# Performance work log

Measured on AMD Instinct MI355X. Metric: run time of the kernel, lower is better.

Reference implementation:

```python
import jax, jax.numpy as jnp
import numpy as np

N = 50000        # nodes
E = 800000       # edges (avg degree 16)
H = 128          # hidden_channels
R = 6            # num_radial
SH = 3           # spin_hidden_channels


def _linear_params(key, out_dim, in_dim):
    # torch Linear default init: U(-1/sqrt(in), 1/sqrt(in)) for weight and bias
    kw, kb = jax.random.split(key)
    bound = 1.0 / np.sqrt(in_dim)
    W = jax.random.uniform(kw, (out_dim, in_dim), minval=-bound, maxval=bound, dtype=jnp.float32)
    b = jax.random.uniform(kb, (out_dim,), minval=-bound, maxval=bound, dtype=jnp.float32)
    return W, b


def setup_inputs() -> dict:
    key = jax.random.key(0)
    ks = jax.random.split(key, 9)
    x = jax.random.randint(ks[0], (N,), 0, 95)                       # atom types
    s = jax.random.randint(ks[1], (N,), 0, 3)                        # spin class in {0,1,2} == (spin + 1)
    rbf = jax.random.normal(ks[2], (E, R), dtype=jnp.float32)
    i = jax.random.randint(ks[3], (E,), 0, N)
    j = jax.random.randint(ks[4], (E,), 0, N)
    emb_w = jax.random.uniform(ks[5], (95, H), minval=-np.sqrt(3), maxval=np.sqrt(3), dtype=jnp.float32)
    spin_w, spin_b = _linear_params(ks[6], SH, 3)
    rbf_w, rbf_b = _linear_params(ks[7], H, R)
    lin_w, lin_b = _linear_params(ks[8], H, 3 * H + 2 * SH)
    return {"x": x, "s": s, "rbf": rbf, "i": i, "j": j,
            "emb_w": emb_w, "spin_w": spin_w, "spin_b": spin_b,
            "rbf_w": rbf_w, "rbf_b": rbf_b, "lin_w": lin_w, "lin_b": lin_b}


def reference(x, s, rbf, i, j, emb_w, spin_w, spin_b, rbf_w, rbf_b, lin_w, lin_b):
    act = jax.nn.silu
    h = emb_w[x]                                              # [N, H] embedding lookup
    spin_oh = jax.nn.one_hot(s, 3, dtype=spin_w.dtype)        # [N, 3]
    spin_feat = spin_oh @ spin_w.T + spin_b                   # [N, SH]
    r = act(rbf @ rbf_w.T + rbf_b)                            # [E, H]
    # concat order matches torch: [x_i, spin_i, x_j, spin_j, rbf]
    feat = jnp.concatenate([h[i], spin_feat[i], h[j], spin_feat[j], r], axis=-1)  # [E, 3H+2SH]
    return act(feat @ lin_w.T + lin_b)                        # [E, H]
```

## Files before the change

### kernel.cpp

```cpp
#include <hip/hip_runtime.h>
#include <hip/hip_bf16.h>

#define NH   128
#define NR   6
#define NCOL 390
#define TILE_E 64
#define LDK  136

typedef __attribute__((ext_vector_type(8))) short bf16x8;
typedef __attribute__((ext_vector_type(4))) float f32x4;

__global__ void prep_tables(const float* __restrict__ emb_w,
                            const float* __restrict__ spin_w,
                            const float* __restrict__ spin_b,
                            const float* __restrict__ lin_w,
                            const float* __restrict__ lin_b,
                            float* __restrict__ Ci, float* __restrict__ Cj) {
    int row = blockIdx.x;
    int n   = threadIdx.x;
    bool isJ = row >= 285;
    int rr = isJ ? row - 285 : row;
    int a  = rr / 3;
    int sc = rr % 3;
    const int col0 = isJ ? 131 : 0;
    const int cols = isJ ? 259 : 128;
    const float* wrow = lin_w + (size_t)n * NCOL;
    float acc = isJ ? 0.0f : lin_b[n];
    #pragma unroll 8
    for (int k = 0; k < NH; ++k)
        acc += emb_w[a * NH + k] * wrow[col0 + k];
    #pragma unroll
    for (int c = 0; c < 3; ++c)
        acc += (spin_w[c * 3 + sc] + spin_b[c]) * wrow[cols + c];
    (isJ ? Cj : Ci)[rr * NH + n] = acc;
}

__global__ void prep_w(const float* __restrict__ lin_w, __hip_bfloat16* __restrict__ Wb) {
    int idx = blockIdx.x * 256 + threadIdx.x;
    int n = idx >> 7, k = idx & 127;
    Wb[idx] = __float2bfloat16(lin_w[(size_t)n * NCOL + 262 + k]);
}

__global__ __launch_bounds__(256, 2) void fused_main(
        const int*   __restrict__ x,   const int* __restrict__ s,
        const float* __restrict__ rbf,
        const int*   __restrict__ gi,  const int* __restrict__ gj,
        const float* __restrict__ rbf_w, const float* __restrict__ rbf_b,
        const float* __restrict__ Ci,  const float* __restrict__ Cj,
        const __hip_bfloat16* __restrict__ Wb,
        float* __restrict__ out, int E) {
    __shared__ __align__(16) __hip_bfloat16 r_lds[TILE_E * LDK];
    __shared__ __align__(16) __hip_bfloat16 w_lds[NH * LDK];
    __shared__ float rbf_lds[TILE_E * NR];
    __shared__ int ci_lds[TILE_E], cj_lds[TILE_E];

    const int tid = threadIdx.x;
    const int e0  = blockIdx.x * TILE_E;

    {
        const uint4* src = (const uint4*)Wb;
        #pragma unroll
        for (int it = 0; it < 8; ++it) {
            int l = it * 256 + tid;
            int row = l >> 4, c = l & 15;
            uint4 v = src[l];
            *(uint4*)&w_lds[row * LDK + c * 8] = v;
        }
    }

    if (tid < 192) {
        int nvalid = (E - e0 >= TILE_E ? TILE_E : (E - e0)) * NR;
        float2 v = make_float2(0.f, 0.f);
        if (tid * 2 < nvalid)
            v = ((const float2*)(rbf + (size_t)e0 * NR))[tid];
        ((float2*)rbf_lds)[tid] = v;
    }

    if (tid < TILE_E) {
        int e = e0 + tid; if (e >= E) e = E - 1;
        int ii = gi[e];
        ci_lds[tid] = x[ii] * 3 + s[ii];
    } else if (tid < 2 * TILE_E) {
        int t = tid - TILE_E;
        int e = e0 + t; if (e >= E) e = E - 1;
        int jj = gj[e];
        cj_lds[t] = x[jj] * 3 + s[jj];
    }
    __syncthreads();

    {
        int k  = tid & 127;
        int hi = tid >> 7;
        float w0 = rbf_w[k * NR + 0], w1 = rbf_w[k * NR + 1], w2 = rbf_w[k * NR + 2];
        float w3 = rbf_w[k * NR + 3], w4 = rbf_w[k * NR + 4], w5 = rbf_w[k * NR + 5];
        float bb = rbf_b[k];
        #pragma unroll 4
        for (int t = 0; t < 32; ++t) {
            int e = t * 2 + hi;
            const float* re = &rbf_lds[e * NR];
            float acc = bb + re[0] * w0 + re[1] * w1 + re[2] * w2
                           + re[3] * w3 + re[4] * w4 + re[5] * w5;
            float sv = acc / (1.0f + __expf(-acc));
            r_lds[e * LDK + k] = __float2bfloat16(sv);
        }
    }
    __syncthreads();

    const int wave   = tid >> 6;
    const int lane   = tid & 63;
    const int lane15 = lane & 15;
    const int quad   = lane >> 4;
    const int e_sub  = wave * 16;

    bf16x8 afrag[4];
    #pragma unroll
    for (int kt = 0; kt < 4; ++kt)
        afrag[kt] = *(const bf16x8*)&r_lds[(e_sub + lane15) * LDK + kt * 32 + quad * 8];

    const int e_row = e_sub + quad * 4;
    int cio[4], cjo[4];
    #pragma unroll
    for (int reg = 0; reg < 4; ++reg) {
        cio[reg] = ci_lds[e_row + reg] * NH;
        cjo[reg] = cj_lds[e_row + reg] * NH;
    }

    #pragma unroll
    for (int nt = 0; nt < 8; ++nt) {
        f32x4 acc = {0.f, 0.f, 0.f, 0.f};
        #pragma unroll
        for (int kt = 0; kt < 4; ++kt) {
            bf16x8 bfrag = *(const bf16x8*)&w_lds[(nt * 16 + lane15) * LDK + kt * 32 + quad * 8];
            acc = __builtin_amdgcn_mfma_f32_16x16x32_bf16(afrag[kt], bfrag, acc, 0, 0, 0);
        }
        int n = nt * 16 + lane15;
        #pragma unroll
        for (int reg = 0; reg < 4; ++reg) {
            int eg = e0 + e_row + reg;
            if (eg < E) {
                float base = Ci[cio[reg] + n] + Cj[cjo[reg] + n];
                float v = acc[reg] + base;
                out[(size_t)eg * NH + n] = v / (1.0f + __expf(-v));
            }
        }
    }
}

extern "C" void kernel_launch(void* const* d_in, const int* in_sizes, int n_in,
                              void* d_out, int out_size, void* d_ws, size_t ws_size,
                              hipStream_t stream) {
    const int*   x      = (const int*)  d_in[0];
    const int*   s      = (const int*)  d_in[1];
    const float* rbf    = (const float*)d_in[2];
    const int*   gi     = (const int*)  d_in[3];
    const int*   gj     = (const int*)  d_in[4];
    const float* emb_w  = (const float*)d_in[5];
    const float* spin_w = (const float*)d_in[6];
    const float* spin_b = (const float*)d_in[7];
    const float* rbf_w  = (const float*)d_in[8];
    const float* rbf_b  = (const float*)d_in[9];
    const float* lin_w  = (const float*)d_in[10];
    const float* lin_b  = (const float*)d_in[11];
    const int E = in_sizes[3];

    float* Ci = (float*)d_ws;
    float* Cj = Ci + 285 * NH;
    __hip_bfloat16* Wb = (__hip_bfloat16*)(Cj + 285 * NH);

    prep_tables<<<570, 128, 0, stream>>>(emb_w, spin_w, spin_b, lin_w, lin_b, Ci, Cj);
    prep_w<<<64, 256, 0, stream>>>(lin_w, Wb);

    int nblk = (E + TILE_E - 1) / TILE_E;
    fused_main<<<nblk, 256, 0, stream>>>(x, s, rbf, gi, gj, rbf_w, rbf_b,
                                         Ci, Cj, Wb, (float*)d_out, E);
}
```

Baseline: 690.4 us.

## Make fused edge kernel persistent with prefetch of next tile's inputs

Converts the main kernel into a persistent grid-stride loop over 128-edge tiles with 512-thread blocks. The bf16 weight tile and rbf weights now load once per block rather than once per tile, and the next tile's rbf values and gathered node indices are prefetched into registers while MFMA and epilogue run. It also uses a reciprocal-based SiLU and nontemporal output stores. Risks are the extra syncs per tile and lower parallelism from a fixed 512-block grid, plus register pressure at 512 threads.

```diff
diff --git a/kernel.cpp b/kernel.cpp
--- a/kernel.cpp
+++ b/kernel.cpp
@@ -4,11 +4,16 @@
 #define NH   128
 #define NR   6
 #define NCOL 390
-#define TILE_E 64
+#define TILE_E 128
 #define LDK  136
+#define NBLK 512
 
 typedef __attribute__((ext_vector_type(8))) short bf16x8;
 typedef __attribute__((ext_vector_type(4))) float f32x4;
+
+__device__ __forceinline__ float fast_silu(float v) {
+    return v * __builtin_amdgcn_rcpf(1.0f + __expf(-v));
+}
 
 __global__ void prep_tables(const float* __restrict__ emb_w,
                             const float* __restrict__ spin_w,
@@ -41,106 +46,122 @@
     Wb[idx] = __float2bfloat16(lin_w[(size_t)n * NCOL + 262 + k]);
 }
 
-__global__ __launch_bounds__(256, 2) void fused_main(
+__global__ __launch_bounds__(512, 4) void fused_main(
         const int*   __restrict__ x,   const int* __restrict__ s,
         const float* __restrict__ rbf,
         const int*   __restrict__ gi,  const int* __restrict__ gj,
         const float* __restrict__ rbf_w, const float* __restrict__ rbf_b,
         const float* __restrict__ Ci,  const float* __restrict__ Cj,
         const __hip_bfloat16* __restrict__ Wb,
-        float* __restrict__ out, int E) {
+        float* __restrict__ out, int E, int ntiles) {
+    __shared__ __align__(16) __hip_bfloat16 w_lds[NH * LDK];
     __shared__ __align__(16) __hip_bfloat16 r_lds[TILE_E * LDK];
-    __shared__ __align__(16) __hip_bfloat16 w_lds[NH * LDK];
     __shared__ float rbf_lds[TILE_E * NR];
     __shared__ int ci_lds[TILE_E], cj_lds[TILE_E];
 
     const int tid = threadIdx.x;
-    const int e0  = blockIdx.x * TILE_E;
+
+    float2 srbf = make_float2(0.f, 0.f);
+    int sci = 0, scj = 0;
+
+    auto load_tile = [&](int tt) {
+        const int en0 = tt * TILE_E;
+        if (tid < 384) {
+            int nval = (E - en0 >= TILE_E ? TILE_E : E - en0) * NR;
+            float2 v = make_float2(0.f, 0.f);
+            if (tid * 2 < nval)
+                v = ((const float2*)(rbf + (size_t)en0 * NR))[tid];
+            srbf = v;
+        }
+        if (tid >= 384) {
+            int e = en0 + (tid - 384); if (e >= E) e = E - 1;
+            int ii = gi[e];
+            sci = x[ii] * 3 + s[ii];
+        }
+        if (tid < 128) {
+            int e = en0 + tid; if (e >= E) e = E - 1;
+            int jj = gj[e];
+            scj = x[jj] * 3 + s[jj];
+        }
+    };
+
+    const int t0 = blockIdx.x;
+    const int gstride = gridDim.x;
+    load_tile(t0);
 
     {
         const uint4* src = (const uint4*)Wb;
         #pragma unroll
-        for (int it = 0; it < 8; ++it) {
-            int l = it * 256 + tid;
-            int row = l >> 4, c = l & 15;
+        for (int it = 0; it < 4; ++it) {
+            int l = it * 512 + tid;
             uint4 v = src[l];
-            *(uint4*)&w_lds[row * LDK + c * 8] = v;
+            *(uint4*)&w_lds[(l >> 4) * LDK + (l & 15) * 8] = v;
         }
     }
 
-    if (tid < 192) {
-        int nvalid = (E - e0 >= TILE_E ? TILE_E : (E - e0)) * NR;
-        float2 v = make_float2(0.f, 0.f);
-        if (tid * 2 < nvalid)
-            v = ((const float2*)(rbf + (size_t)e0 * NR))[tid];
-        ((float2*)rbf_lds)[tid] = v;
-    }
-
-    if (tid < TILE_E) {
-        int e = e0 + tid; if (e >= E) e = E - 1;
-        int ii = gi[e];
-        ci_lds[tid] = x[ii] * 3 + s[ii];
-    } else if (tid < 2 * TILE_E) {
-        int t = tid - TILE_E;
-        int e = e0 + t; if (e >= E) e = E - 1;
-        int jj = gj[e];
-        cj_lds[t] = x[jj] * 3 + s[jj];
-    }
-    __syncthreads();
-
-    {
-        int k  = tid & 127;
-        int hi = tid >> 7;
-        float w0 = rbf_w[k * NR + 0], w1 = rbf_w[k * NR + 1], w2 = rbf_w[k * NR + 2];
-        float w3 = rbf_w[k * NR + 3], w4 = rbf_w[k * NR + 4], w5 = rbf_w[k * NR + 5];
-        float bb = rbf_b[k];
-        #pragma unroll 4
-        for (int t = 0; t < 32; ++t) {
-            int e = t * 2 + hi;
-            const float* re = &rbf_lds[e * NR];
-            float acc = bb + re[0] * w0 + re[1] * w1 + re[2] * w2
-                           + re[3] * w3 + re[4] * w4 + re[5] * w5;
-            float sv = acc / (1.0f + __expf(-acc));
-            r_lds[e * LDK + k] = __float2bfloat16(sv);
-        }
-    }
-    __syncthreads();
+    const int kk = tid & 127;
+    const int hi = tid >> 7;
+    const float w0 = rbf_w[kk * NR + 0], w1 = rbf_w[kk * NR + 1], w2 = rbf_w[kk * NR + 2];
+    const float w3 = rbf_w[kk * NR + 3], w4 = rbf_w[kk * NR + 4], w5 = rbf_w[kk * NR + 5];
+    const float bb = rbf_b[kk];
 
     const int wave   = tid >> 6;
     const int lane   = tid & 63;
     const int lane15 = lane & 15;
     const int quad   = lane >> 4;
     const int e_sub  = wave * 16;
+    const int e_row  = e_sub + quad * 4;
 
-    bf16x8 afrag[4];
-    #pragma unroll
-    for (int kt = 0; kt < 4; ++kt)
-        afrag[kt] = *(const bf16x8*)&r_lds[(e_sub + lane15) * LDK + kt * 32 + quad * 8];
+    for (int t = t0; t < ntiles; t += gstride) {
+        __syncthreads();
+        if (tid < 384) ((float2*)rbf_lds)[tid] = srbf;
+        if (tid >= 384) ci_lds[tid - 384] = sci;
+        if (tid < 128)  cj_lds[tid] = scj;
+        __syncthreads();
 
-    const int e_row = e_sub + quad * 4;
-    int cio[4], cjo[4];
-    #pragma unroll
-    for (int reg = 0; reg < 4; ++reg) {
-        cio[reg] = ci_lds[e_row + reg] * NH;
-        cjo[reg] = cj_lds[e_row + reg] * NH;
-    }
+        #pragma unroll 4
+        for (int it = 0; it < 32; ++it) {
+            int e = it * 4 + hi;
+            const float* re = &rbf_lds[e * NR];
+            float a = bb + re[0] * w0 + re[1] * w1 + re[2] * w2
+                         + re[3] * w3 + re[4] * w4 + re[5] * w5;
+            r_lds[e * LDK + kk] = __float2bfloat16(fast_silu(a));
+        }
+        __syncthreads();
 
-    #pragma unroll
-    for (int nt = 0; nt < 8; ++nt) {
-        f32x4 acc = {0.f, 0.f, 0.f, 0.f};
+        bf16x8 afrag[4];
         #pragma unroll
-        for (int kt = 0; kt < 4; ++kt) {
-            bf16x8 bfrag = *(const bf16x8*)&w_lds[(nt * 16 + lane15) * LDK + kt * 32 + quad * 8];
-            acc = __builtin_amdgcn_mfma_f32_16x16x32_bf16(afrag[kt], bfrag, acc, 0, 0, 0);
-        }
-        int n = nt * 16 + lane15;
+        for (int kt = 0; kt < 4; ++kt)
+            afrag[kt] = *(const bf16x8*)&r_lds[(e_sub + lane15) * LDK + kt * 32 + quad * 8];
+
+        const int e0 = t * TILE_E;
+        const float* cip[4]; const float* cjp[4]; float* op[4];
         #pragma unroll
         for (int reg = 0; reg < 4; ++reg) {
-            int eg = e0 + e_row + reg;
-            if (eg < E) {
-                float base = Ci[cio[reg] + n] + Cj[cjo[reg] + n];
+            cip[reg] = Ci + ci_lds[e_row + reg] * NH + lane15;
+            cjp[reg] = Cj + cj_lds[e_row + reg] * NH + lane15;
+            op[reg]  = out + (size_t)(e0 + e_row + reg) * NH + lane15;
+        }
+        const bool tail = (e0 + TILE_E > E);
+
+        int tn = t + gstride;
+        if (tn < ntiles) load_tile(tn);
+
+        #pragma unroll
+        for (int nt = 0; nt < 8; ++nt) {
+            f32x4 acc = {0.f, 0.f, 0.f, 0.f};
+            #pragma unroll
+            for (int kt = 0; kt < 4; ++kt) {
+                bf16x8 bfrag = *(const bf16x8*)&w_lds[(nt * 16 + lane15) * LDK + kt * 32 + quad * 8];
+                acc = __builtin_amdgcn_mfma_f32_16x16x32_bf16(afrag[kt], bfrag, acc, 0, 0, 0);
+            }
+            #pragma unroll
+            for (int reg = 0; reg < 4; ++reg) {
+                float base = cip[reg][nt * 16] + cjp[reg][nt * 16];
                 float v = acc[reg] + base;
-                out[(size_t)eg * NH + n] = v / (1.0f + __expf(-v));
+                float sv = fast_silu(v);
+                if (!tail || (e0 + e_row + reg < E))
+                    __builtin_nontemporal_store(sv, op[reg] + nt * 16);
             }
         }
     }
@@ -170,7 +191,8 @@
     prep_tables<<<570, 128, 0, stream>>>(emb_w, spin_w, spin_b, lin_w, lin_b, Ci, Cj);
     prep_w<<<64, 256, 0, stream>>>(lin_w, Wb);
 
-    int nblk = (E + TILE_E - 1) / TILE_E;
-    fused_main<<<nblk, 256, 0, stream>>>(x, s, rbf, gi, gj, rbf_w, rbf_b,
-                                         Ci, Cj, Wb, (float*)d_out, E);
+    int ntiles = (E + TILE_E - 1) / TILE_E;
+    int nblk = ntiles < NBLK ? ntiles : NBLK;
+    fused_main<<<nblk, 512, 0, stream>>>(x, s, rbf, gi, gj, rbf_w, rbf_b,
+                                         Ci, Cj, Wb, (float*)d_out, E, ntiles);
 }
```

New measurement: 553.9 us. -19.8%, faster.
